# Optimization experiments

Measured on AMD Instinct MI355X. Metric: run time of the kernel, lower is better.

The kernel has to match this reference:

```python
import jax, jax.numpy as jnp
import numpy as np

MAXLEN = 20
NLAYERS = 4


def setup_inputs() -> dict:
    key = jax.random.key(0)
    ks = jax.random.split(key, 16)
    B, SRC, H, V = 256, 64, 1024, 32000
    s = 1.0 / np.sqrt(H)
    return {
        "encoder_outputs": jax.random.normal(ks[0], (B, SRC, H), jnp.float32),
        "encoder_hidden": jax.random.normal(ks[1], (NLAYERS, B, H), jnp.float32),
        "emb_table": jax.random.normal(ks[2], (V, H), jnp.float32) * s,
        "gru_w_ih": jax.random.normal(ks[3], (NLAYERS, 3 * H, H), jnp.float32) * s,
        "gru_w_hh": jax.random.normal(ks[4], (NLAYERS, 3 * H, H), jnp.float32) * s,
        "gru_b_ih": jax.random.normal(ks[5], (NLAYERS, 3 * H), jnp.float32) * s,
        "gru_b_hh": jax.random.normal(ks[6], (NLAYERS, 3 * H), jnp.float32) * s,
        "out_w": jax.random.normal(ks[7], (V, H), jnp.float32) * s,
        "out_b": jax.random.normal(ks[8], (V,), jnp.float32) * s,
        "l1_w": jax.random.normal(ks[9], (3, 2 * H), jnp.float32) * s,
        "l1_b": jax.random.normal(ks[10], (3,), jnp.float32) * s,
        "l2_w": jax.random.normal(ks[11], (1, 3), jnp.float32),
        "l2_b": jax.random.normal(ks[12], (1,), jnp.float32),
    }


def _gru_layer(x, h, w_ih, w_hh, b_ih, b_hh):
    # PyTorch GRU gate order: r, z, n
    gi = x @ w_ih.T + b_ih  # [B, 3H]
    gh = h @ w_hh.T + b_hh  # [B, 3H]
    i_r, i_z, i_n = jnp.split(gi, 3, axis=-1)
    h_r, h_z, h_n = jnp.split(gh, 3, axis=-1)
    r = jax.nn.sigmoid(i_r + h_r)
    z = jax.nn.sigmoid(i_z + h_z)
    n = jnp.tanh(i_n + r * h_n)
    return (1.0 - z) * n + z * h


def reference(encoder_outputs, encoder_hidden, emb_table, gru_w_ih, gru_w_hh,
              gru_b_ih, gru_b_hh, out_w, out_b, l1_w, l1_b, l2_w, l2_b):
    B = encoder_outputs.shape[0]
    enc_h0 = encoder_hidden[0]  # [B, H]

    def step(carry, _):
        h, tok = carry  # h: [4,B,H], tok: [B] int32
        # attention-score branch (computed in torch but unused -> DCE'd by jit)
        a = jnp.broadcast_to(h[0, -1], enc_h0.shape)
        enc = jnp.concatenate([a, enc_h0], axis=1)  # [B, 2H]
        _align = jax.nn.softmax((enc @ l1_w.T + l1_b) @ l2_w.T + l2_b, axis=0)
        # embedding + relu + 4-layer GRU (seq len 1)
        x = jax.nn.relu(emb_table[tok])  # [B, H]
        hs = []
        for l in range(NLAYERS):
            hl = _gru_layer(x, h[l], gru_w_ih[l], gru_w_hh[l], gru_b_ih[l], gru_b_hh[l])
            hs.append(hl)
            x = hl
        h = jnp.stack(hs)  # [4, B, H]
        logits = x @ out_w.T + out_b  # [B, V]
        tok = jnp.argmax(logits, axis=-1).astype(jnp.int32)  # greedy (topk(1))
        return (h, tok), logits

    tok0 = jnp.zeros((B,), jnp.int32)
    (h_final, _), logits = jax.lax.scan(step, (encoder_hidden, tok0), None, length=MAXLEN)
    # [T,B,V] -> [B,T,V], then log_softmax over vocab
    log_probs = jax.nn.log_softmax(jnp.transpose(logits, (1, 0, 2)), axis=-1)
    return log_probs, h_final
```

## Files before the change

### kernel.cpp

```cpp
#include <hip/hip_runtime.h>
#include <math.h>

#define HD 1024
#define NBATCH 256
#define VOC 32000
#define TSTEPS 20
#define OUT_ROW 640000LL
#define BH ((size_t)NBATCH * HD)
#define NCHUNK 500
#define THR 0.125f

typedef _Float16 f16;
typedef __attribute__((ext_vector_type(4))) _Float16 f16x4;
typedef __attribute__((ext_vector_type(8))) _Float16 f16x8;
typedef __attribute__((ext_vector_type(4))) float f32x4;

#define GLOBAL_AS __attribute__((address_space(1)))
#define LDS_AS    __attribute__((address_space(3)))

static __device__ __forceinline__ float sigmoidf_(float v) {
  return 1.0f / (1.0f + expf(-v));
}


__global__ void f32_to_f16_k(const float* __restrict__ in, f16* __restrict__ out, long n8) {
  long i = (long)blockIdx.x * 256 + threadIdx.x;
  long stride = (long)gridDim.x * 256;
  for (; i < n8; i += stride) {
    float4 a = *((const float4*)in + i * 2);
    float4 b = *((const float4*)in + i * 2 + 1);
    f16x8 o;
    o[0] = (f16)a.x; o[1] = (f16)a.y; o[2] = (f16)a.z; o[3] = (f16)a.w;
    o[4] = (f16)b.x; o[5] = (f16)b.y; o[6] = (f16)b.z; o[7] = (f16)b.w;
    *((f16x8*)out + i) = o;
  }
}

__global__ void split_f32_k(const float* __restrict__ in, f16* __restrict__ hi,
                            f16* __restrict__ lo, long n8) {
  long i = (long)blockIdx.x * 256 + threadIdx.x;
  long stride = (long)gridDim.x * 256;
  for (; i < n8; i += stride) {
    float4 a = *((const float4*)in + i * 2);
    float4 b = *((const float4*)in + i * 2 + 1);
    float v[8] = {a.x, a.y, a.z, a.w, b.x, b.y, b.z, b.w};
    f16x8 h8, l8;
    #pragma unroll
    for (int j = 0; j < 8; ++j) {
      f16 h = (f16)v[j];
      h8[j] = h;
      l8[j] = (f16)(v[j] - (float)h);
    }
    *((f16x8*)hi + i) = h8;
    *((f16x8*)lo + i) = l8;
  }
}

__global__ __launch_bounds__(256)
void gemm_gru_mfma4_k(const f16* __restrict__ a0_hi, const f16* __restrict__ a0_lo,
                      const f16* __restrict__ a1_hi, const f16* __restrict__ a1_lo,
                      const float* __restrict__ emb, const int* __restrict__ tok, int use_emb,
                      const float* __restrict__ w_ih, const float* __restrict__ w_hh,
                      float* __restrict__ gg2) {
  __shared__ f16x8 atoms[2][1088];

  const int tid = threadIdx.x;
  const int lane = tid & 63;
  const int wave = tid >> 6;
  const int wm = wave >> 1, wn = wave & 1;
  const int l15 = lane & 15, l4 = lane >> 4;
  const int n0g = blockIdx.x * 64;
  const int m0 = blockIdx.y * 64;
  const int kb = blockIdx.z * 512;

  const f16 *ahi, *alo; const float* W; int nc;
  if (n0g < 3072) { ahi = a0_hi; alo = a0_lo; W = w_ih; nc = n0g; }
  else            { ahi = a1_hi; alo = a1_lo; W = w_hh; nc = n0g - 3072; }
  const bool embmode = use_emb && (n0g < 3072);

  f32x4 acc[2][2];
  #pragma unroll
  for (int mi = 0; mi < 2; ++mi)
    #pragma unroll
    for (int ni = 0; ni < 2; ++ni) acc[mi][ni] = (f32x4){0.f, 0.f, 0.f, 0.f};

  const int sr = tid >> 2, skg = tid & 3;
  const int satom = skg * 68 + sr;
  const float* wgp = W + (size_t)(nc + sr) * HD + kb + skg * 8;
  const f16* agh = ahi + (size_t)(m0 + sr) * HD + kb + skg * 8;
  const f16* agl = alo + (size_t)(m0 + sr) * HD + kb + skg * 8;
  const float* egp = embmode ? (emb + (size_t)tok[m0 + sr] * HD + kb + skg * 8) : wgp;

  #define LOADREGS(k0, rah, ral, wbh, wbl) { \
    if (embmode) { \
      float4 e0 = *(const float4*)(egp + (k0)); \
      float4 e1 = *(const float4*)(egp + (k0) + 4); \
      float av[8] = {fmaxf(e0.x,0.f), fmaxf(e0.y,0.f), fmaxf(e0.z,0.f), fmaxf(e0.w,0.f), \
                     fmaxf(e1.x,0.f), fmaxf(e1.y,0.f), fmaxf(e1.z,0.f), fmaxf(e1.w,0.f)}; \
      _Pragma("unroll") \
      for (int j = 0; j < 8; ++j) { \
        f16 h = (f16)av[j]; rah[j] = h; ral[j] = (f16)(av[j] - (float)h); \
      } \
    } else { \
      rah = *(const f16x8*)(agh + (k0)); \
      ral = *(const f16x8*)(agl + (k0)); \
    } \
    float4 w0 = *(const float4*)(wgp + (k0)); \
    float4 w1 = *(const float4*)(wgp + (k0) + 4); \
    float wv[8] = {w0.x, w0.y, w0.z, w0.w, w1.x, w1.y, w1.z, w1.w}; \
    _Pragma("unroll") \
    for (int j = 0; j < 8; ++j) { \
      f16 h = (f16)wv[j]; wbh[j] = h; wbl[j] = (f16)(wv[j] - (float)h); \
    } }

  {
    f16x8 rah, ral, wbh, wbl;
    LOADREGS(0, rah, ral, wbh, wbl);
    atoms[0][satom]       = rah;
    atoms[0][272 + satom] = ral;
    atoms[0][544 + satom] = wbh;
    atoms[0][816 + satom] = wbl;
  }
  __syncthreads();

  for (int kt = 0; kt < 16; ++kt) {
    const int cur = kt & 1;
    f16x8 nah, nal, nbh, nbl;
    if (kt < 15) { LOADREGS((kt + 1) * 32, nah, nal, nbh, nbl); }

    f16x8 fah[2], fal[2], fbh[2], fbl[2];
    #pragma unroll
    for (int mi = 0; mi < 2; ++mi) {
      int idx = l4 * 68 + wm * 32 + mi * 16 + l15;
      fah[mi] = atoms[cur][idx];
      fal[mi] = atoms[cur][272 + idx];
    }
    #pragma unroll
    for (int ni = 0; ni < 2; ++ni) {
      int idx = l4 * 68 + wn * 32 + ni * 16 + l15;
      fbh[ni] = atoms[cur][544 + idx];
      fbl[ni] = atoms[cur][816 + idx];
    }
    #pragma unroll
    for (int mi = 0; mi < 2; ++mi)
      #pragma unroll
      for (int ni = 0; ni < 2; ++ni) {
        acc[mi][ni] = __builtin_amdgcn_mfma_f32_16x16x32_f16(fah[mi], fbh[ni], acc[mi][ni], 0, 0, 0);
        acc[mi][ni] = __builtin_amdgcn_mfma_f32_16x16x32_f16(fah[mi], fbl[ni], acc[mi][ni], 0, 0, 0);
        acc[mi][ni] = __builtin_amdgcn_mfma_f32_16x16x32_f16(fal[mi], fbh[ni], acc[mi][ni], 0, 0, 0);
      }

    if (kt < 15) {
      atoms[cur ^ 1][satom]       = nah;
      atoms[cur ^ 1][272 + satom] = nal;
      atoms[cur ^ 1][544 + satom] = nbh;
      atoms[cur ^ 1][816 + satom] = nbl;
    }
    __syncthreads();
  }
  #undef LOADREGS

  float* outp = gg2 + (size_t)blockIdx.z * NBATCH * 6144;
  #pragma unroll
  for (int mi = 0; mi < 2; ++mi)
    #pragma unroll
    for (int ni = 0; ni < 2; ++ni) {
      const int col = n0g + wn * 32 + ni * 16 + l15;
      #pragma unroll
      for (int r = 0; r < 4; ++r) {
        const int row = m0 + wm * 32 + mi * 16 + l4 * 4 + r;
        outp[(size_t)row * 6144 + col] = acc[mi][ni][r];
      }
    }
}

static __device__ __forceinline__ float4 add4_(float4 a, float4 b) {
  float4 r; r.x = a.x + b.x; r.y = a.y + b.y; r.z = a.z + b.z; r.w = a.w + b.w; return r;
}
__global__ void gru_gates_split2_k(const float* __restrict__ gg2,
                                   const float* __restrict__ b_ih, const float* __restrict__ b_hh,
                                   const f16* __restrict__ hold_hi, const f16* __restrict__ hold_lo,
                                   f16* __restrict__ hnew_hi, f16* __restrict__ hnew_lo) {
  int idx = blockIdx.x * 256 + threadIdx.x;
  int b = idx >> 8;
  int k4 = (idx & 255) << 2;
  const float* g0 = gg2 + (size_t)b * 6144;
  const float* g1 = gg2 + (size_t)NBATCH * 6144 + (size_t)b * 6144;
  #define LD2(off) add4_(*(const float4*)(g0 + (off) + k4), *(const float4*)(g1 + (off) + k4))
  float4 gir = LD2(0);
  float4 giz = LD2(1024);
  float4 gin = LD2(2048);
  float4 ghr = LD2(3072);
  float4 ghz = LD2(4096);
  float4 ghn = LD2(5120);
  #undef LD2
  float4 bir = *(const float4*)(b_ih + k4);
  float4 biz = *(const float4*)(b_ih + 1024 + k4);
  float4 bin = *(const float4*)(b_ih + 2048 + k4);
  float4 bhr = *(const float4*)(b_hh + k4);
  float4 bhz = *(const float4*)(b_hh + 1024 + k4);
  float4 bhn = *(const float4*)(b_hh + 2048 + k4);
  f16x4 hh = *(const f16x4*)(hold_hi + (size_t)b * HD + k4);
  f16x4 hl = *(const f16x4*)(hold_lo + (size_t)b * HD + k4);
  float hov[4];
  #pragma unroll
  for (int j = 0; j < 4; ++j) hov[j] = (float)hh[j] + (float)hl[j];
  float4 ho; ho.x = hov[0]; ho.y = hov[1]; ho.z = hov[2]; ho.w = hov[3];
  float4 o;
  #define GATE(c) { \
    float rr = sigmoidf_(gir.c + bir.c + ghr.c + bhr.c); \
    float zz = sigmoidf_(giz.c + biz.c + ghz.c + bhz.c); \
    float nn = tanhf(gin.c + bin.c + rr * (ghn.c + bhn.c)); \
    o.c = (1.0f - zz) * nn + zz * ho.c; }
  GATE(x) GATE(y) GATE(z) GATE(w)
  #undef GATE
  float vv[4] = {o.x, o.y, o.z, o.w};
  f16x4 h4, l4;
  #pragma unroll
  for (int j = 0; j < 4; ++j) {
    f16 h = (f16)vv[j];
    h4[j] = h;
    l4[j] = (f16)(vv[j] - (float)h);
  }
  *(f16x4*)(hnew_hi + (size_t)b * HD + k4) = h4;
  *(f16x4*)(hnew_lo + (size_t)b * HD + k4) = l4;
}

__global__ __launch_bounds__(256)
void gemm_logits3_k(const f16* __restrict__ xf, const f16* __restrict__ wf,
                    const float* __restrict__ bias, float* __restrict__ out,
                    float* __restrict__ pmax, float* __restrict__ psum) {
  __shared__ f16 lb[2][2112];
  const int tid = threadIdx.x;
  const int lane = tid & 63;
  const int wave = tid >> 6;
  const int l15 = lane & 15, l4 = lane >> 4;
  const int chunk = blockIdx.x;
  const int n0 = chunk * 64;

  f32x4 acc[4][4];
  #pragma unroll
  for (int mi = 0; mi < 4; ++mi)
    #pragma unroll
    for (int ni = 0; ni < 4; ++ni) acc[mi][ni] = (f32x4){0.f, 0.f, 0.f, 0.f};

  f16x8 a_cur[4], a_nxt[4];

  #define STAGE(k0, buf) { \
    const f16* src = wf + (size_t)(n0 + lane) * 1024 + (k0) + wave * 8; \
    __builtin_amdgcn_global_load_lds((const GLOBAL_AS void*)src, \
        (LDS_AS void*)(lb[buf] + wave * 528), 16, 0, 0); }
  #define LOADA(k0, dst) { \
    _Pragma("unroll") \
    for (int mi = 0; mi < 4; ++mi) { \
      int row = wave * 64 + mi * 16 + l15; \
      dst[mi] = *(const f16x8*)(xf + (size_t)row * 1024 + (k0) + l4 * 8); \
    } }

  STAGE(0, 0);
  LOADA(0, a_cur);
  __syncthreads();

  for (int kt = 0; kt < 32; ++kt) {
    const int cur = kt & 1;
    f16x8 b[4];
    #pragma unroll
    for (int ni = 0; ni < 4; ++ni)
      b[ni] = *(const f16x8*)(lb[cur] + (size_t)l4 * 528 + (size_t)(ni * 16 + l15) * 8);
    if (kt < 31) {
      STAGE((kt + 1) * 32, cur ^ 1);
      LOADA((kt + 1) * 32, a_nxt);
    }
    #pragma unroll
    for (int mi = 0; mi < 4; ++mi)
      #pragma unroll
      for (int ni = 0; ni < 4; ++ni)
        acc[mi][ni] = __builtin_amdgcn_mfma_f32_16x16x32_f16(a_cur[mi], b[ni], acc[mi][ni], 0, 0, 0);
    __syncthreads();
    #pragma unroll
    for (int mi = 0; mi < 4; ++mi) a_cur[mi] = a_nxt[mi];
  }
  #undef STAGE
  #undef LOADA

  float bv[4];
  #pragma unroll
  for (int ni = 0; ni < 4; ++ni) bv[ni] = bias[n0 + ni * 16 + l15];

  #pragma unroll
  for (int mi = 0; mi < 4; ++mi) {
    #pragma unroll
    for (int r = 0; r < 4; ++r) {
      const int row = wave * 64 + mi * 16 + l4 * 4 + r;
      float v[4];
      #pragma unroll
      for (int ni = 0; ni < 4; ++ni) {
        v[ni] = acc[mi][ni][r] + bv[ni];
        out[(size_t)row * OUT_ROW + n0 + ni * 16 + l15] = v[ni];
      }
      float m = fmaxf(fmaxf(v[0], v[1]), fmaxf(v[2], v[3]));
      #pragma unroll
      for (int d = 1; d < 16; d <<= 1) m = fmaxf(m, __shfl_xor(m, d, 64));
      float s = __expf(v[0] - m) + __expf(v[1] - m) + __expf(v[2] - m) + __expf(v[3] - m);
      #pragma unroll
      for (int d = 1; d < 16; d <<= 1) s += __shfl_xor(s, d, 64);
      if (l15 == 0) {
        pmax[(size_t)row * NCHUNK + chunk] = m;
        psum[(size_t)row * NCHUNK + chunk] = s;
      }
    }
  }
}

__global__ __launch_bounds__(256)
void token_k(const float* __restrict__ pmax, const float* __restrict__ psum,
             const float* __restrict__ lg,
             const f16* __restrict__ xhi, const f16* __restrict__ xlo,
             const float* __restrict__ w, const float* __restrict__ ob,
             float* __restrict__ lse_out, int* __restrict__ tok) {
  __shared__ float sm[256];
  __shared__ float ssum[256];
  __shared__ double sd[256];
  __shared__ int sfl[16];
  __shared__ int scand[32];
  __shared__ int sflc, scnt;
  const int b = blockIdx.x;
  const int tid = threadIdx.x;
  const float* PM = pmax + (size_t)b * NCHUNK;
  const float* PS = psum + (size_t)b * NCHUNK;

  float m = -3.4e38f, s = 0.0f;
  for (int c = tid; c < NCHUNK; c += 256) {
    float mc = PM[c], sc = PS[c];
    float M = fmaxf(m, mc);
    s = s * __expf(m - M) + sc * __expf(mc - M);
    m = M;
  }
  sm[tid] = m; ssum[tid] = s;
  if (tid == 0) { sflc = 0; scnt = 0; }
  __syncthreads();
  for (int off = 128; off; off >>= 1) {
    if (tid < off) {
      float m1 = sm[tid], m2 = sm[tid + off];
      float M = fmaxf(m1, m2);
      ssum[tid] = ssum[tid] * __expf(m1 - M) + ssum[tid + off] * __expf(m2 - M);
      sm[tid] = M;
    }
    __syncthreads();
  }
  const float gmax = sm[0];
  const float lse = gmax + logf(ssum[0]);
  if (tid == 0) lse_out[b] = lse;
  const float thr = gmax - THR;

  for (int c = tid; c < NCHUNK; c += 256) {
    if (PM[c] >= thr) {
      int p = atomicAdd(&sflc, 1);
      if (p < 16) sfl[p] = c;
    }
  }
  __syncthreads();
  const int nf = sflc < 16 ? sflc : 16;

  const int g = tid >> 6, li = tid & 63;
  for (int f0 = 0; f0 < nf; f0 += 4) {
    int f = f0 + g;
    if (f < nf) {
      float v = lg[(size_t)b * OUT_ROW + sfl[f] * 64 + li];
      if (v >= thr) {
        int p = atomicAdd(&scnt, 1);
        if (p < 32) scand[p] = sfl[f] * 64 + li;
      }
    }
  }
  __syncthreads();
  const int c = scnt < 32 ? scnt : 32;

  if (c == 1) {
    if (tid == 0) tok[b] = scand[0];
    return;
  }

  double best = -1.0e300; int bi = 0x7fffffff;
  for (int j = 0; j < c; ++j) {
    const int idx = scand[j];
    double p = 0.0;
    const f16* xh = xhi + (size_t)b * HD;
    const f16* xl = xlo + (size_t)b * HD;
    const float* wr = w + (size_t)idx * HD;
    for (int k = tid; k < HD; k += 256)
      p += ((double)xh[k] + (double)xl[k]) * (double)wr[k];
    sd[tid] = p;
    __syncthreads();
    for (int off = 128; off; off >>= 1) {
      if (tid < off) sd[tid] += sd[tid + off];
      __syncthreads();
    }
    if (tid == 0) sd[0] += (double)ob[idx];
    __syncthreads();
    double tot = sd[0];
    if (tot > best || (tot == best && idx < bi)) { best = tot; bi = idx; }
    __syncthreads();
  }
  if (tid == 0) tok[b] = bi;
}

__global__ void sub_all_k(float* __restrict__ out, const float* __restrict__ lse_all) {
  const long total = (long)NBATCH * TSTEPS * (VOC / 4);
  long i = (long)blockIdx.x * 256 + threadIdx.x;
  const long stride = (long)gridDim.x * 256;
  for (; i < total; i += stride) {
    long b = i / (TSTEPS * (VOC / 4));
    long r = i - b * (TSTEPS * (VOC / 4));
    long t = r / (VOC / 4);
    float l = lse_all[t * NBATCH + b];
    float4 v = ((float4*)out)[i];
    v.x -= l; v.y -= l; v.z -= l; v.w -= l;
    ((float4*)out)[i] = v;
  }
}

__global__ void combine_h_k(const f16* __restrict__ hi, const f16* __restrict__ lo,
                            float* __restrict__ o, int n4) {
  int i = blockIdx.x * 256 + threadIdx.x;
  if (i >= n4) return;
  f16x4 h = ((const f16x4*)hi)[i];
  f16x4 l = ((const f16x4*)lo)[i];
  float4 v;
  v.x = (float)h[0] + (float)l[0];
  v.y = (float)h[1] + (float)l[1];
  v.z = (float)h[2] + (float)l[2];
  v.w = (float)h[3] + (float)l[3];
  ((float4*)o)[i] = v;
}

extern "C" void kernel_launch(void* const* d_in, const int* in_sizes, int n_in,
                              void* d_out, int out_size, void* d_ws, size_t ws_size,
                              hipStream_t stream) {
  (void)in_sizes; (void)n_in; (void)out_size;
  const float* enc_hidden = (const float*)d_in[1];
  const float* emb   = (const float*)d_in[2];
  const float* w_ih  = (const float*)d_in[3];
  const float* w_hh  = (const float*)d_in[4];
  const float* b_ih  = (const float*)d_in[5];
  const float* b_hh  = (const float*)d_in[6];
  const float* out_w = (const float*)d_in[7];
  const float* out_b = (const float*)d_in[8];
  float* out = (float*)d_out;

  size_t off = 0;
  char* base = (char*)d_ws;
  #define WSALLOC(bytes) ((void*)(base + off)); off += (((size_t)(bytes)) + 255) & ~(size_t)255
  float* gg2     = (float*) WSALLOC((size_t)2 * NBATCH * 6144 * 4);
  f16*   hs_hi   = (f16*)   WSALLOC(2 * 4 * BH * 2);
  f16*   hs_lo   = (f16*)   WSALLOC(2 * 4 * BH * 2);
  int*   tok     = (int*)   WSALLOC(1024);
  float* pmax    = (float*) WSALLOC((size_t)NBATCH * NCHUNK * 4);
  float* psum    = (float*) WSALLOC((size_t)NBATCH * NCHUNK * 4);
  float* lse_all = (float*) WSALLOC((size_t)TSTEPS * NBATCH * 4);
  f16*   wf16    = (f16*)   WSALLOC((size_t)VOC * HD * 2);
  #undef WSALLOC
  if (off > ws_size) return;

  f32_to_f16_k<<<2048, 256, 0, stream>>>(out_w, wf16, (long)VOC * HD / 8);
  split_f32_k<<<512, 256, 0, stream>>>(enc_hidden, hs_hi, hs_lo, (long)(4 * BH / 8));
  hipMemsetAsync(tok, 0, NBATCH * 4, stream);

  int p = 0;
  for (int t = 0; t < TSTEPS; ++t) {
    f16* hp_hi = hs_hi + (size_t)p * 4 * BH;
    f16* hp_lo = hs_lo + (size_t)p * 4 * BH;
    f16* hn_hi = hs_hi + (size_t)(1 - p) * 4 * BH;
    f16* hn_lo = hs_lo + (size_t)(1 - p) * 4 * BH;

    for (int l = 0; l < 4; ++l) {
      const f16* a0hi = (l == 0) ? hs_hi : hn_hi + (size_t)(l - 1) * BH;
      const f16* a0lo = (l == 0) ? hs_lo : hn_lo + (size_t)(l - 1) * BH;
      gemm_gru_mfma4_k<<<dim3(96, 4, 2), 256, 0, stream>>>(
          a0hi, a0lo, hp_hi + (size_t)l * BH, hp_lo + (size_t)l * BH,
          emb, tok, (l == 0) ? 1 : 0,
          w_ih + (size_t)l * 3072 * HD, w_hh + (size_t)l * 3072 * HD, gg2);
      gru_gates_split2_k<<<256, 256, 0, stream>>>(
          gg2, b_ih + l * 3072, b_hh + l * 3072,
          hp_hi + (size_t)l * BH, hp_lo + (size_t)l * BH,
          hn_hi + (size_t)l * BH, hn_lo + (size_t)l * BH);
    }

    float* lg = out + (size_t)t * VOC;
    gemm_logits3_k<<<NCHUNK, 256, 0, stream>>>(
        hn_hi + (size_t)3 * BH, wf16, out_b, lg, pmax, psum);
    token_k<<<NBATCH, 256, 0, stream>>>(
        pmax, psum, lg, hn_hi + (size_t)3 * BH, hn_lo + (size_t)3 * BH,
        out_w, out_b, lse_all + (size_t)t * NBATCH, tok);

    p ^= 1;
  }

  sub_all_k<<<16384, 256, 0, stream>>>(out, lse_all);

  combine_h_k<<<1024, 256, 0, stream>>>(hs_hi, hs_lo,
                                        out + (size_t)NBATCH * TSTEPS * VOC,
                                        (int)(4 * BH / 4));
}
```

Before: 3.995 ms.

## Pre-tile and pre-split GRU and output weights into MFMA-ready f16 tiles

Adds a one-time preprocessing kernel that converts the f32 GRU weights into hi/lo f16 pairs stored in contiguous 64x32 tiles, and retiles the output projection weights the same way. The GRU GEMM then streams weights straight to LDS with global_load_lds instead of reconverting f32 weights on every step, and reads activations directly from global memory into registers. The logits GEMM uses the tiled layout for contiguous 2KB loads. This costs extra workspace for the hi/lo weight copies and a larger setup pass.

```diff
diff --git a/kernel.cpp b/kernel.cpp
--- a/kernel.cpp
+++ b/kernel.cpp
@@ -20,20 +20,6 @@
 
 static __device__ __forceinline__ float sigmoidf_(float v) {
   return 1.0f / (1.0f + expf(-v));
-}
-
-
-__global__ void f32_to_f16_k(const float* __restrict__ in, f16* __restrict__ out, long n8) {
-  long i = (long)blockIdx.x * 256 + threadIdx.x;
-  long stride = (long)gridDim.x * 256;
-  for (; i < n8; i += stride) {
-    float4 a = *((const float4*)in + i * 2);
-    float4 b = *((const float4*)in + i * 2 + 1);
-    f16x8 o;
-    o[0] = (f16)a.x; o[1] = (f16)a.y; o[2] = (f16)a.z; o[3] = (f16)a.w;
-    o[4] = (f16)b.x; o[5] = (f16)b.y; o[6] = (f16)b.z; o[7] = (f16)b.w;
-    *((f16x8*)out + i) = o;
-  }
 }
 
 __global__ void split_f32_k(const float* __restrict__ in, f16* __restrict__ hi,
@@ -56,14 +42,41 @@
   }
 }
 
+__global__ void tile_f16_k(const float* __restrict__ src, f16* __restrict__ thi,
+                           f16* __restrict__ tlo) {
+  __shared__ f16x8 lh[256];
+  __shared__ f16x8 ll[256];
+  const int bid = blockIdx.x;
+  const int tid = threadIdx.x;
+  const int r = tid >> 2, kg = tid & 3;
+  const size_t rb = bid >> 5;
+  const int ktg = bid & 31;
+  const float* sp = src + (rb * 64 + r) * 1024 + ktg * 32 + kg * 8;
+  float4 a = *(const float4*)sp;
+  float4 b = *(const float4*)(sp + 4);
+  float v[8] = {a.x, a.y, a.z, a.w, b.x, b.y, b.z, b.w};
+  f16x8 h8, l8;
+  #pragma unroll
+  for (int j = 0; j < 8; ++j) {
+    f16 h = (f16)v[j];
+    h8[j] = h;
+    l8[j] = (f16)(v[j] - (float)h);
+  }
+  lh[kg * 64 + r] = h8;
+  ll[kg * 64 + r] = l8;
+  __syncthreads();
+  *((f16x8*)(thi + (size_t)bid * 2048) + tid) = lh[tid];
+  if (tlo) *((f16x8*)(tlo + (size_t)bid * 2048) + tid) = ll[tid];
+}
+
 __global__ __launch_bounds__(256)
-void gemm_gru_mfma4_k(const f16* __restrict__ a0_hi, const f16* __restrict__ a0_lo,
+void gemm_gru_mfma5_k(const f16* __restrict__ a0_hi, const f16* __restrict__ a0_lo,
                       const f16* __restrict__ a1_hi, const f16* __restrict__ a1_lo,
                       const float* __restrict__ emb, const int* __restrict__ tok, int use_emb,
-                      const float* __restrict__ w_ih, const float* __restrict__ w_hh,
+                      const f16* __restrict__ whi_t, const f16* __restrict__ wlo_t, int layer,
                       float* __restrict__ gg2) {
-  __shared__ f16x8 atoms[2][1088];
-
+  __shared__ f16 lbh[2][2112];
+  __shared__ f16 lbl[2][2112];
   const int tid = threadIdx.x;
   const int lane = tid & 63;
   const int wave = tid >> 6;
@@ -71,11 +84,14 @@
   const int l15 = lane & 15, l4 = lane >> 4;
   const int n0g = blockIdx.x * 64;
   const int m0 = blockIdx.y * 64;
-  const int kb = blockIdx.z * 512;
-
-  const f16 *ahi, *alo; const float* W; int nc;
-  if (n0g < 3072) { ahi = a0_hi; alo = a0_lo; W = w_ih; nc = n0g; }
-  else            { ahi = a1_hi; alo = a1_lo; W = w_hh; nc = n0g - 3072; }
+  const int z = blockIdx.z;
+  const int kb = z * 512;
+
+  const f16 *ahi, *alo; int nc; size_t tile0;
+  if (n0g < 3072) { ahi = a0_hi; alo = a0_lo; nc = n0g;
+                    tile0 = (size_t)(layer * 48 + (nc >> 6)) * 32 + z * 16; }
+  else            { ahi = a1_hi; alo = a1_lo; nc = n0g - 3072;
+                    tile0 = 6144 + (size_t)(layer * 48 + (nc >> 6)) * 32 + z * 16; }
   const bool embmode = use_emb && (n0g < 3072);
 
   f32x4 acc[2][2];
@@ -84,62 +100,54 @@
     #pragma unroll
     for (int ni = 0; ni < 2; ++ni) acc[mi][ni] = (f32x4){0.f, 0.f, 0.f, 0.f};
 
-  const int sr = tid >> 2, skg = tid & 3;
-  const int satom = skg * 68 + sr;
-  const float* wgp = W + (size_t)(nc + sr) * HD + kb + skg * 8;
-  const f16* agh = ahi + (size_t)(m0 + sr) * HD + kb + skg * 8;
-  const f16* agl = alo + (size_t)(m0 + sr) * HD + kb + skg * 8;
-  const float* egp = embmode ? (emb + (size_t)tok[m0 + sr] * HD + kb + skg * 8) : wgp;
-
-  #define LOADREGS(k0, rah, ral, wbh, wbl) { \
-    if (embmode) { \
-      float4 e0 = *(const float4*)(egp + (k0)); \
-      float4 e1 = *(const float4*)(egp + (k0) + 4); \
-      float av[8] = {fmaxf(e0.x,0.f), fmaxf(e0.y,0.f), fmaxf(e0.z,0.f), fmaxf(e0.w,0.f), \
-                     fmaxf(e1.x,0.f), fmaxf(e1.y,0.f), fmaxf(e1.z,0.f), fmaxf(e1.w,0.f)}; \
-      _Pragma("unroll") \
-      for (int j = 0; j < 8; ++j) { \
-        f16 h = (f16)av[j]; rah[j] = h; ral[j] = (f16)(av[j] - (float)h); \
-      } \
-    } else { \
-      rah = *(const f16x8*)(agh + (k0)); \
-      ral = *(const f16x8*)(agl + (k0)); \
-    } \
-    float4 w0 = *(const float4*)(wgp + (k0)); \
-    float4 w1 = *(const float4*)(wgp + (k0) + 4); \
-    float wv[8] = {w0.x, w0.y, w0.z, w0.w, w1.x, w1.y, w1.z, w1.w}; \
-    _Pragma("unroll") \
-    for (int j = 0; j < 8; ++j) { \
-      f16 h = (f16)wv[j]; wbh[j] = h; wbl[j] = (f16)(wv[j] - (float)h); \
-    } }
-
-  {
-    f16x8 rah, ral, wbh, wbl;
-    LOADREGS(0, rah, ral, wbh, wbl);
-    atoms[0][satom]       = rah;
-    atoms[0][272 + satom] = ral;
-    atoms[0][544 + satom] = wbh;
-    atoms[0][816 + satom] = wbl;
-  }
+  const int arow0 = m0 + wm * 32 + l15;
+  const f16* ap_h = ahi + (size_t)arow0 * HD + kb + l4 * 8;
+  const f16* ap_l = alo + (size_t)arow0 * HD + kb + l4 * 8;
+  const float* ep0 = embmode ? (emb + (size_t)tok[arow0] * HD + kb + l4 * 8) : (const float*)0;
+  const float* ep1 = embmode ? (emb + (size_t)tok[arow0 + 16] * HD + kb + l4 * 8) : (const float*)0;
+
+  #define STAGE(kt, buf) { \
+    const f16* sh = whi_t + (tile0 + (kt)) * 2048 + wave * 512 + lane * 8; \
+    __builtin_amdgcn_global_load_lds((const GLOBAL_AS void*)sh, \
+        (LDS_AS void*)(lbh[buf] + wave * 528), 16, 0, 0); \
+    const f16* sl = wlo_t + (tile0 + (kt)) * 2048 + wave * 512 + lane * 8; \
+    __builtin_amdgcn_global_load_lds((const GLOBAL_AS void*)sl, \
+        (LDS_AS void*)(lbl[buf] + wave * 528), 16, 0, 0); }
+
+  STAGE(0, 0);
   __syncthreads();
 
   for (int kt = 0; kt < 16; ++kt) {
     const int cur = kt & 1;
-    f16x8 nah, nal, nbh, nbl;
-    if (kt < 15) { LOADREGS((kt + 1) * 32, nah, nal, nbh, nbl); }
+    if (kt < 15) STAGE(kt + 1, cur ^ 1);
 
     f16x8 fah[2], fal[2], fbh[2], fbl[2];
-    #pragma unroll
-    for (int mi = 0; mi < 2; ++mi) {
-      int idx = l4 * 68 + wm * 32 + mi * 16 + l15;
-      fah[mi] = atoms[cur][idx];
-      fal[mi] = atoms[cur][272 + idx];
+    if (embmode) {
+      #pragma unroll
+      for (int mi = 0; mi < 2; ++mi) {
+        const float* ep = mi ? ep1 : ep0;
+        float4 e0 = *(const float4*)(ep + kt * 32);
+        float4 e1 = *(const float4*)(ep + kt * 32 + 4);
+        float av[8] = {fmaxf(e0.x,0.f), fmaxf(e0.y,0.f), fmaxf(e0.z,0.f), fmaxf(e0.w,0.f),
+                       fmaxf(e1.x,0.f), fmaxf(e1.y,0.f), fmaxf(e1.z,0.f), fmaxf(e1.w,0.f)};
+        #pragma unroll
+        for (int j = 0; j < 8; ++j) {
+          f16 h = (f16)av[j];
+          fah[mi][j] = h;
+          fal[mi][j] = (f16)(av[j] - (float)h);
+        }
+      }
+    } else {
+      fah[0] = *(const f16x8*)(ap_h + kt * 32);
+      fah[1] = *(const f16x8*)(ap_h + (size_t)16 * HD + kt * 32);
+      fal[0] = *(const f16x8*)(ap_l + kt * 32);
+      fal[1] = *(const f16x8*)(ap_l + (size_t)16 * HD + kt * 32);
     }
     #pragma unroll
     for (int ni = 0; ni < 2; ++ni) {
-      int idx = l4 * 68 + wn * 32 + ni * 16 + l15;
-      fbh[ni] = atoms[cur][544 + idx];
-      fbl[ni] = atoms[cur][816 + idx];
+      const int off = l4 * 528 + (wn * 32 + ni * 16 + l15) * 8;
+      fbh[ni] = *(const f16x8*)(lbh[cur] + off);
+      fbl[ni] = *(const f16x8*)(lbl[cur] + off);
     }
     #pragma unroll
     for (int mi = 0; mi < 2; ++mi)
@@ -149,16 +157,9 @@
         acc[mi][ni] = __builtin_amdgcn_mfma_f32_16x16x32_f16(fah[mi], fbl[ni], acc[mi][ni], 0, 0, 0);
         acc[mi][ni] = __builtin_amdgcn_mfma_f32_16x16x32_f16(fal[mi], fbh[ni], acc[mi][ni], 0, 0, 0);
       }
-
-    if (kt < 15) {
-      atoms[cur ^ 1][satom]       = nah;
-      atoms[cur ^ 1][272 + satom] = nal;
-      atoms[cur ^ 1][544 + satom] = nbh;
-      atoms[cur ^ 1][816 + satom] = nbl;
-    }
     __syncthreads();
   }
-  #undef LOADREGS
+  #undef STAGE
 
   float* outp = gg2 + (size_t)blockIdx.z * NBATCH * 6144;
   #pragma unroll
@@ -227,7 +228,7 @@
 }
 
 __global__ __launch_bounds__(256)
-void gemm_logits3_k(const f16* __restrict__ xf, const f16* __restrict__ wf,
+void gemm_logits4_k(const f16* __restrict__ xf, const f16* __restrict__ wft,
                     const float* __restrict__ bias, float* __restrict__ out,
                     float* __restrict__ pmax, float* __restrict__ psum) {
   __shared__ f16 lb[2][2112];
@@ -246,8 +247,8 @@
 
   f16x8 a_cur[4], a_nxt[4];
 
-  #define STAGE(k0, buf) { \
-    const f16* src = wf + (size_t)(n0 + lane) * 1024 + (k0) + wave * 8; \
+  #define STAGE(kt, buf) { \
+    const f16* src = wft + ((size_t)chunk * 32 + (kt)) * 2048 + wave * 512 + lane * 8; \
     __builtin_amdgcn_global_load_lds((const GLOBAL_AS void*)src, \
         (LDS_AS void*)(lb[buf] + wave * 528), 16, 0, 0); }
   #define LOADA(k0, dst) { \
@@ -268,7 +269,7 @@
     for (int ni = 0; ni < 4; ++ni)
       b[ni] = *(const f16x8*)(lb[cur] + (size_t)l4 * 528 + (size_t)(ni * 16 + l15) * 8);
     if (kt < 31) {
-      STAGE((kt + 1) * 32, cur ^ 1);
+      STAGE(kt + 1, cur ^ 1);
       LOADA((kt + 1) * 32, a_nxt);
     }
     #pragma unroll
@@ -458,11 +459,16 @@
   float* pmax    = (float*) WSALLOC((size_t)NBATCH * NCHUNK * 4);
   float* psum    = (float*) WSALLOC((size_t)NBATCH * NCHUNK * 4);
   float* lse_all = (float*) WSALLOC((size_t)TSTEPS * NBATCH * 4);
-  f16*   wf16    = (f16*)   WSALLOC((size_t)VOC * HD * 2);
+  f16*   wft     = (f16*)   WSALLOC((size_t)VOC * HD * 2);
+  f16*   whi_t   = (f16*)   WSALLOC((size_t)2 * 4 * 3072 * HD * 2);
+  f16*   wlo_t   = (f16*)   WSALLOC((size_t)2 * 4 * 3072 * HD * 2);
   #undef WSALLOC
   if (off > ws_size) return;
 
-  f32_to_f16_k<<<2048, 256, 0, stream>>>(out_w, wf16, (long)VOC * HD / 8);
+  tile_f16_k<<<16000, 256, 0, stream>>>(out_w, wft, (f16*)0);
+  tile_f16_k<<<6144, 256, 0, stream>>>(w_ih, whi_t, wlo_t);
+  tile_f16_k<<<6144, 256, 0, stream>>>(w_hh, whi_t + (size_t)6144 * 2048,
+                                       wlo_t + (size_t)6144 * 2048);
   split_f32_k<<<512, 256, 0, stream>>>(enc_hidden, hs_hi, hs_lo, (long)(4 * BH / 8));
   hipMemsetAsync(tok, 0, NBATCH * 4, stream);
 
@@ -476,10 +482,10 @@
     for (int l = 0; l < 4; ++l) {
       const f16* a0hi = (l == 0) ? hs_hi : hn_hi + (size_t)(l - 1) * BH;
       const f16* a0lo = (l == 0) ? hs_lo : hn_lo + (size_t)(l - 1) * BH;
-      gemm_gru_mfma4_k<<<dim3(96, 4, 2), 256, 0, stream>>>(
+      gemm_gru_mfma5_k<<<dim3(96, 4, 2), 256, 0, stream>>>(
           a0hi, a0lo, hp_hi + (size_t)l * BH, hp_lo + (size_t)l * BH,
           emb, tok, (l == 0) ? 1 : 0,
-          w_ih + (size_t)l * 3072 * HD, w_hh + (size_t)l * 3072 * HD, gg2);
+          whi_t, wlo_t, l, gg2);
       gru_gates_split2_k<<<256, 256, 0, stream>>>(
           gg2, b_ih + l * 3072, b_hh + l * 3072,
           hp_hi + (size_t)l * BH, hp_lo + (size_t)l * BH,
@@ -487,8 +493,8 @@
     }
 
     float* lg = out + (size_t)t * VOC;
-    gemm_logits3_k<<<NCHUNK, 256, 0, stream>>>(
-        hn_hi + (size_t)3 * BH, wf16, out_b, lg, pmax, psum);
+    gemm_logits4_k<<<NCHUNK, 256, 0, stream>>>(
+        hn_hi + (size_t)3 * BH, wft, out_b, lg, pmax, psum);
     token_k<<<NBATCH, 256, 0, stream>>>(
         pmax, psum, lg, hn_hi + (size_t)3 * BH, hn_lo + (size_t)3 * BH,
         out_w, out_b, lse_all + (size_t)t * NBATCH, tok);
```

Result: slower. 4.787 ms (+19.8%).
